# Kernel optimization log

Measured on AMD Instinct MI355X. Metric: run time of the kernel, lower is better.

## Reference

```python
import jax, jax.numpy as jnp
import numpy as np

GRID_DIM = 32      # output crop size
RES = 0.25         # A per voxel
CUBES = 5          # cubes_around_atoms_dim
NUM_CH = 5
BOX = 20.0         # dumb coords pin extents to [-20, 20]^3
LATO = 2 * CUBES + 1                      # 11
D = int(2 * BOX / RES) + 2 * (CUBES + 1) + 1  # 173, static full grid dim


def setup_inputs() -> dict:
    key = jax.random.key(0)
    k1, k2 = jax.random.split(key)
    B, N = 8, 64
    coords = jax.random.uniform(k1, (B, N, 3), jnp.float32, -7.5, 7.5)
    atoms_channel = jax.random.randint(k2, (B, N), 0, NUM_CH).astype(jnp.int32)
    radius = jnp.full((B, N), 0.5, jnp.float32)
    return {"coords": coords, "atoms_channel": atoms_channel, "radius": radius}


def _add_dumb_coords(coords, atoms_channel, radius):
    B = coords.shape[0]
    coords = jnp.concatenate(
        [coords, jnp.full((B, 1, 3), -BOX, coords.dtype), jnp.full((B, 1, 3), BOX, coords.dtype)], axis=1)
    atoms_channel = jnp.concatenate([atoms_channel, jnp.zeros((B, 2), atoms_channel.dtype)], axis=1)
    radius = jnp.concatenate([radius, jnp.full((B, 2), 0.5, radius.dtype)], axis=1)
    return coords, atoms_channel, radius


def reference(coords, atoms_channel, radius):
    coords, atoms_channel, radius = _add_dumb_coords(coords, atoms_channel, radius)
    B, M, _ = coords.shape
    # coordinates in voxel units; translation puts min corner at CUBES+1 cells
    scaled = (coords + BOX) / RES + (CUBES + 1)            # [B,M,3]
    base = jnp.floor(scaled).astype(jnp.int32)             # host voxel of each atom
    r = np.arange(-CUBES, CUBES + 1)
    off = jnp.asarray(np.stack(np.meshgrid(r, r, r, indexing='ij'), -1).reshape(-1, 3), jnp.int32)  # [K,3]
    cell = base[:, :, None, :] + off[None, None]           # [B,M,K,3] grid cells touched
    # squared distance (in A^2) from atom to cell centers; avoids sqrt (smooth at 0)
    delta = scaled[:, :, None, :] - (cell.astype(jnp.float32) + 0.5)
    d2 = jnp.sum(delta * delta, axis=-1) * (RES * RES)     # [B,M,K]
    # gaussian splat: exp(-d^2 / (2 r^2))
    val = jnp.exp(-0.5 * d2 / (radius[:, :, None] ** 2))   # [B,M,K]
    b_idx = jnp.arange(B, dtype=jnp.int32)[:, None, None]
    ch = atoms_channel[:, :, None].astype(jnp.int32)
    flat = (((b_idx * NUM_CH + ch) * D + cell[..., 0]) * D + cell[..., 1]) * D + cell[..., 2]
    vol = jnp.zeros((B * NUM_CH * D * D * D,), jnp.float32)
    vol = vol.at[flat.reshape(-1)].add(val.reshape(-1), mode='drop')
    vol = vol.reshape(B, NUM_CH, D, D, D)
    c = D // 2
    lo, hi = c - GRID_DIM // 2, c + GRID_DIM // 2
    return vol[:, :, lo:hi, lo:hi, lo:hi]
```

## Files before the change

kernel.cpp:

```cpp
#include <hip/hip_runtime.h>

#define NUM_CH     5
#define GRID_DIM   32
#define VOX_PER_B  (GRID_DIM*GRID_DIM*GRID_DIM)

__global__ __launch_bounds__(256) void gather_kernel(
    const float* __restrict__ coords,
    const int*   __restrict__ channel,
    const float* __restrict__ radius,
    float* __restrict__ out)
{
    const int blk  = blockIdx.x & 127;
    const int b    = blockIdx.x >> 7;
    const int lin  = (blk << 8) | threadIdx.x;
    const int lane = threadIdx.x & 63;

    const int a0i = (b << 6) + lane;
    const float vsx = (coords[3*a0i + 0] + 20.0f) * 4.0f - 64.0f;
    const float vsy = (coords[3*a0i + 1] + 20.0f) * 4.0f - 64.0f;
    const float vsz = (coords[3*a0i + 2] + 20.0f) * 4.0f - 64.0f;
    const float rr  = radius[a0i];
    const float vkg = -0.03125f / (rr * rr);
    const int   vch = channel[a0i];

    const int gx  = blk >> 2;
    const int gy0 = (blk & 3) << 3;
    const float fx = (float)gx + 0.5f;
    const float fy = (float)(((lin >> 5) & 31)) + 0.5f;
    const float fz = (float)(lin & 31) + 0.5f;

    const bool cand = fabsf(vsx - fx) <= 5.5f &&
                      fabsf(vsy - ((float)gy0 + 4.0f)) <= 9.0f &&
                      fabsf(vsz - 16.0f) <= 21.0f;
    unsigned long long mask = __ballot(cand);

    float c0 = 0.f, c1 = 0.f, c2 = 0.f, c3 = 0.f, c4 = 0.f;

    while (mask) {
        const int a = __ffsll(mask) - 1;
        mask &= mask - 1;
        const float sx = __int_as_float(__builtin_amdgcn_readlane(__float_as_int(vsx), a));
        const float sy = __int_as_float(__builtin_amdgcn_readlane(__float_as_int(vsy), a));
        const float sz = __int_as_float(__builtin_amdgcn_readlane(__float_as_int(vsz), a));
        const float dx = fx - sx;
        const float dy = fy - sy;
        const float dz = fz - sz;
        if (fmaxf(fabsf(dy), fabsf(dz)) <= 5.5f) {
            const float kg = __int_as_float(__builtin_amdgcn_readlane(__float_as_int(vkg), a));
            const float val = __expf(kg * (dx*dx + dy*dy + dz*dz));
            const int ch = __builtin_amdgcn_readlane(vch, a);
            if      (ch == 0) c0 += val;
            else if (ch == 1) c1 += val;
            else if (ch == 2) c2 += val;
            else if (ch == 3) c3 += val;
            else              c4 += val;
        }
    }

    float* o = out + (size_t)b * NUM_CH * VOX_PER_B + lin;
    o[0*VOX_PER_B] = c0;
    o[1*VOX_PER_B] = c1;
    o[2*VOX_PER_B] = c2;
    o[3*VOX_PER_B] = c3;
    o[4*VOX_PER_B] = c4;
}

extern "C" void kernel_launch(void* const* d_in, const int* in_sizes, int n_in,
                              void* d_out, int out_size, void* d_ws, size_t ws_size,
                              hipStream_t stream) {
    const float* coords  = (const float*)d_in[0];
    const int*   channel = (const int*)d_in[1];
    const float* radius  = (const float*)d_in[2];
    float* out = (float*)d_out;

    const int B = in_sizes[1] / 64;
    hipLaunchKernelGGL(gather_kernel, dim3(B * 128), dim3(256), 0, stream,
                       coords, channel, radius, out);
}
```

Measured before the change: 59.75 us.

## Compute four z-voxels per thread with float4 stores and fewer blocks

Each thread now covers four consecutive z voxels in one x-slab instead of one voxel, so the grid shrinks fourfold. The readlane broadcasts and the dy test are shared across the four voxels, and each channel is written with a float4 store. In exchange each thread holds more accumulator registers and runs four exps per candidate atom. Wave-level candidate culling is coarser in z (a wave spans 8 y rows by all 32 z), so more masked-out exps may be computed, and fewer waves are available to hide latency.

```diff
diff --git a/kernel.cpp b/kernel.cpp
--- a/kernel.cpp
+++ b/kernel.cpp
@@ -10,10 +10,12 @@
     const float* __restrict__ radius,
     float* __restrict__ out)
 {
-    const int blk  = blockIdx.x & 127;
-    const int b    = blockIdx.x >> 7;
-    const int lin  = (blk << 8) | threadIdx.x;
-    const int lane = threadIdx.x & 63;
+    const int b    = blockIdx.x >> 5;
+    const int gx   = blockIdx.x & 31;
+    const int tid  = threadIdx.x;
+    const int lane = tid & 63;
+    const int gy   = tid >> 3;
+    const int gz0  = (tid & 7) << 2;
 
     const int a0i = (b << 6) + lane;
     const float vsx = (coords[3*a0i + 0] + 20.0f) * 4.0f - 64.0f;
@@ -23,46 +25,57 @@
     const float vkg = -0.03125f / (rr * rr);
     const int   vch = channel[a0i];
 
-    const int gx  = blk >> 2;
-    const int gy0 = (blk & 3) << 3;
-    const float fx = (float)gx + 0.5f;
-    const float fy = (float)(((lin >> 5) & 31)) + 0.5f;
-    const float fz = (float)(lin & 31) + 0.5f;
+    const float fx  = (float)gx + 0.5f;
+    const float fy  = (float)gy + 0.5f;
+    const float fz0 = (float)gz0 + 0.5f;
+    const float wyc = (float)((tid >> 6) << 3) + 4.0f;
 
     const bool cand = fabsf(vsx - fx) <= 5.5f &&
-                      fabsf(vsy - ((float)gy0 + 4.0f)) <= 9.0f &&
+                      fabsf(vsy - wyc) <= 9.0f &&
                       fabsf(vsz - 16.0f) <= 21.0f;
     unsigned long long mask = __ballot(cand);
 
-    float c0 = 0.f, c1 = 0.f, c2 = 0.f, c3 = 0.f, c4 = 0.f;
+    float4 c0 = make_float4(0.f,0.f,0.f,0.f);
+    float4 c1 = c0, c2 = c0, c3 = c0, c4 = c0;
 
     while (mask) {
         const int a = __ffsll(mask) - 1;
         mask &= mask - 1;
-        const float sx = __int_as_float(__builtin_amdgcn_readlane(__float_as_int(vsx), a));
         const float sy = __int_as_float(__builtin_amdgcn_readlane(__float_as_int(vsy), a));
-        const float sz = __int_as_float(__builtin_amdgcn_readlane(__float_as_int(vsz), a));
-        const float dx = fx - sx;
         const float dy = fy - sy;
-        const float dz = fz - sz;
-        if (fmaxf(fabsf(dy), fabsf(dz)) <= 5.5f) {
+        if (fabsf(dy) <= 5.5f) {
+            const float sx = __int_as_float(__builtin_amdgcn_readlane(__float_as_int(vsx), a));
+            const float sz = __int_as_float(__builtin_amdgcn_readlane(__float_as_int(vsz), a));
             const float kg = __int_as_float(__builtin_amdgcn_readlane(__float_as_int(vkg), a));
-            const float val = __expf(kg * (dx*dx + dy*dy + dz*dz));
-            const int ch = __builtin_amdgcn_readlane(vch, a);
-            if      (ch == 0) c0 += val;
-            else if (ch == 1) c1 += val;
-            else if (ch == 2) c2 += val;
-            else if (ch == 3) c3 += val;
-            else              c4 += val;
+            const int   ch = __builtin_amdgcn_readlane(vch, a);
+            const float dx  = fx - sx;
+            const float b2  = dx*dx + dy*dy;
+            const float dz0 = fz0 - sz;
+            const float dz1 = dz0 + 1.0f;
+            const float dz2 = dz0 + 2.0f;
+            const float dz3 = dz0 + 3.0f;
+            float v0 = __expf(kg * (b2 + dz0*dz0));
+            float v1 = __expf(kg * (b2 + dz1*dz1));
+            float v2 = __expf(kg * (b2 + dz2*dz2));
+            float v3 = __expf(kg * (b2 + dz3*dz3));
+            v0 = (fabsf(dz0) <= 5.5f) ? v0 : 0.0f;
+            v1 = (fabsf(dz1) <= 5.5f) ? v1 : 0.0f;
+            v2 = (fabsf(dz2) <= 5.5f) ? v2 : 0.0f;
+            v3 = (fabsf(dz3) <= 5.5f) ? v3 : 0.0f;
+            if      (ch == 0) { c0.x += v0; c0.y += v1; c0.z += v2; c0.w += v3; }
+            else if (ch == 1) { c1.x += v0; c1.y += v1; c1.z += v2; c1.w += v3; }
+            else if (ch == 2) { c2.x += v0; c2.y += v1; c2.z += v2; c2.w += v3; }
+            else if (ch == 3) { c3.x += v0; c3.y += v1; c3.z += v2; c3.w += v3; }
+            else              { c4.x += v0; c4.y += v1; c4.z += v2; c4.w += v3; }
         }
     }
 
-    float* o = out + (size_t)b * NUM_CH * VOX_PER_B + lin;
-    o[0*VOX_PER_B] = c0;
-    o[1*VOX_PER_B] = c1;
-    o[2*VOX_PER_B] = c2;
-    o[3*VOX_PER_B] = c3;
-    o[4*VOX_PER_B] = c4;
+    float* o = out + (size_t)b * NUM_CH * VOX_PER_B + (gx << 10) + (gy << 5) + gz0;
+    *reinterpret_cast<float4*>(o + 0*VOX_PER_B) = c0;
+    *reinterpret_cast<float4*>(o + 1*VOX_PER_B) = c1;
+    *reinterpret_cast<float4*>(o + 2*VOX_PER_B) = c2;
+    *reinterpret_cast<float4*>(o + 3*VOX_PER_B) = c3;
+    *reinterpret_cast<float4*>(o + 4*VOX_PER_B) = c4;
 }
 
 extern "C" void kernel_launch(void* const* d_in, const int* in_sizes, int n_in,
@@ -74,6 +87,6 @@
     float* out = (float*)d_out;
 
     const int B = in_sizes[1] / 64;
-    hipLaunchKernelGGL(gather_kernel, dim3(B * 128), dim3(256), 0, stream,
+    hipLaunchKernelGGL(gather_kernel, dim3(B * 32), dim3(256), 0, stream,
                        coords, channel, radius, out);
 }
```

New measurement: 60.45 us. Within noise of the previous version (+1.2%).
